# Kernel optimization log

Measured on AMD Instinct MI355X. Metric: run time of the kernel, lower is better.

The kernel has to match this reference:

```python
import jax, jax.numpy as jnp
import numpy as np

NUM_NODES = 256
IN_FEAT = 64
HIDDEN = 512
N_CLASSES = 2
BATCH = 256


def setup_inputs() -> dict:
    key = jax.random.key(0)
    ks = jax.random.split(key, 10)
    return {
        "z": jax.random.normal(ks[0], (BATCH, 1, NUM_NODES, NUM_NODES), dtype=jnp.float32),
        "node_emb": jax.random.normal(ks[1], (NUM_NODES, IN_FEAT), dtype=jnp.float32),
        "w1": jax.random.normal(ks[2], (IN_FEAT, HIDDEN), dtype=jnp.float32) * (1.0 / np.sqrt(IN_FEAT)),
        "b1": jnp.zeros((HIDDEN,), dtype=jnp.float32),
        "w2": jax.random.normal(ks[3], (HIDDEN, HIDDEN), dtype=jnp.float32) * (1.0 / np.sqrt(HIDDEN)),
        "b2": jnp.zeros((HIDDEN,), dtype=jnp.float32),
        "w3": jax.random.normal(ks[4], (HIDDEN, HIDDEN), dtype=jnp.float32) * (1.0 / np.sqrt(HIDDEN)),
        "b3": jnp.zeros((HIDDEN,), dtype=jnp.float32),
        "fcw": jax.random.normal(ks[5], (HIDDEN, N_CLASSES), dtype=jnp.float32) * (1.0 / np.sqrt(HIDDEN)),
        "fcb": jnp.zeros((N_CLASSES,), dtype=jnp.float32),
    }


def reference(z, node_emb, w1, b1, w2, b2, w3, b3, fcw, fcb):
    # z: (B, 1, N, N) latent interpreted as weighted adjacency
    z_sq = jnp.squeeze(z, axis=1)                         # (B, N, N)
    A = jax.nn.sigmoid(z_sq)
    A = (A + jnp.swapaxes(A, 1, 2)) * 0.5                  # symmetrize
    A_hat = A + jnp.eye(A.shape[-1], dtype=A.dtype)[None]  # add self loops
    D_hat = jnp.sum(A_hat, axis=2) + 1e-6                  # (B, N) degrees
    d_inv_sqrt = D_hat ** -0.5
    # norm_A = D^{-1/2} A_hat D^{-1/2} via row/col scaling (same math as diag bmm)
    norm_A = A_hat * d_inv_sqrt[:, :, None] * d_inv_sqrt[:, None, :]

    X = jnp.broadcast_to(node_emb[None], (z.shape[0],) + node_emb.shape)  # (B, N, F)
    H1 = jax.nn.relu(jnp.einsum('bij,bjh->bih', norm_A, X @ w1 + b1))
    H2 = jax.nn.relu(jnp.einsum('bij,bjh->bih', norm_A, H1 @ w2 + b2))
    H3 = jax.nn.relu(jnp.einsum('bij,bjh->bih', norm_A, H2 @ w3 + b3))
    graph_emb = jnp.mean(H3, axis=1)                       # (B, H)
    logits = graph_emb @ fcw + fcb                         # (B, n_classes)
    return logits
```

## Files before the change

kernel.cpp:

```cpp
#include <hip/hip_runtime.h>
#include <stdint.h>

#define B_ 256
#define N_ 256
#define F_ 64
#define H_ 512

typedef _Float16 f16;
typedef _Float16 f16x8 __attribute__((ext_vector_type(8)));
typedef _Float16 f16x4 __attribute__((ext_vector_type(4)));
typedef float    f32x4 __attribute__((ext_vector_type(4)));

__device__ __forceinline__ float sigmoidf_(float x) {
    return 1.0f / (1.0f + __expf(-x));
}

__global__ __launch_bounds__(256) void k_sums(const float* __restrict__ z,
                                              f16* __restrict__ S,
                                              float* __restrict__ R,
                                              float* __restrict__ Cpart) {
    int b = blockIdx.y, c = blockIdx.x;
    int tid = threadIdx.x, lane = tid & 63, w = tid >> 6;
    float colacc[4] = {0.f, 0.f, 0.f, 0.f};
    for (int r = 0; r < 16; r++) {
        int i = c * 64 + w * 16 + r;
        size_t base = ((size_t)(b * N_ + i)) * N_;
        float4 v = *(const float4*)(z + base + lane * 4);
        float s0 = sigmoidf_(v.x), s1 = sigmoidf_(v.y),
              s2 = sigmoidf_(v.z), s3 = sigmoidf_(v.w);
        f16x4 sv = { (f16)s0, (f16)s1, (f16)s2, (f16)s3 };
        *(f16x4*)(S + base + lane * 4) = sv;
        colacc[0] += s0; colacc[1] += s1; colacc[2] += s2; colacc[3] += s3;
        float rs = s0 + s1 + s2 + s3;
        for (int off = 32; off; off >>= 1) rs += __shfl_down(rs, off, 64);
        if (lane == 0) R[b * N_ + i] = rs;
    }
    __shared__ float cbuf[4][N_];
    #pragma unroll
    for (int k = 0; k < 4; k++) cbuf[w][lane * 4 + k] = colacc[k];
    __syncthreads();
    float s4 = cbuf[0][tid] + cbuf[1][tid] + cbuf[2][tid] + cbuf[3][tid];
    Cpart[((size_t)c * B_ + b) * N_ + tid] = s4;
}

__global__ __launch_bounds__(256) void k_norma3(const f16* __restrict__ S,
                                                const float* __restrict__ R,
                                                const float* __restrict__ Cpart,
                                                f16* __restrict__ nA) {
    __shared__ f16 T0[128 * 129];
    __shared__ f16 T1[128 * 129];
    __shared__ float Dv[N_];
    int b = blockIdx.y, t = blockIdx.x;
    int tid = threadIdx.x;
    const f16* Sb = S + (size_t)b * N_ * N_;
    f16* Ab = nA + (size_t)b * N_ * N_;

    float cs = Cpart[(size_t)b * N_ + tid]
             + Cpart[((size_t)B_ + b) * N_ + tid]
             + Cpart[((size_t)2 * B_ + b) * N_ + tid]
             + Cpart[((size_t)3 * B_ + b) * N_ + tid];
    Dv[tid] = rsqrtf(1.0f + 1e-6f + 0.5f * (R[b * N_ + tid] + cs));

    auto stage = [&](const f16* src, f16* dst) {
        #pragma unroll
        for (int it = 0; it < 8; it++) {
            int u = it * 256 + tid;
            int r = u >> 4, c8 = (u & 15) * 8;
            *(f16x8*)&dst[r * 129 + c8] = *(const f16x8*)&src[(size_t)r * N_ + c8];
        }
    };
    if (t == 0)      stage(Sb, T0);
    else if (t == 1) stage(Sb + 128 * N_ + 128, T0);
    else           { stage(Sb + 128, T0); stage(Sb + (size_t)128 * N_, T1); }
    __syncthreads();

    auto emit = [&](const f16* Dir, const f16* Mir, int i0, int j0) {
        #pragma unroll
        for (int it = 0; it < 8; it++) {
            int il = it * 16 + (tid >> 4), jl8 = (tid & 15) * 8;
            float di = Dv[i0 + il];
            f16x8 d = *(const f16x8*)&Dir[il * 129 + jl8];
            f16x8 o;
            #pragma unroll
            for (int k = 0; k < 8; k++) {
                float v = 0.5f * ((float)d[k] + (float)Mir[(jl8 + k) * 129 + il]);
                if (i0 + il == j0 + jl8 + k) v += 1.0f;
                o[k] = (f16)(v * di * Dv[j0 + jl8 + k]);
            }
            *(f16x8*)&Ab[(size_t)(i0 + il) * N_ + j0 + jl8] = o;
        }
    };
    if (t == 0)      emit(T0, T0, 0, 0);
    else if (t == 1) emit(T0, T0, 128, 128);
    else           { emit(T0, T1, 0, 128); emit(T1, T0, 128, 0); }
}

__global__ __launch_bounds__(256) void k_prep(const float* __restrict__ ne,
                                              const float* __restrict__ w1,
                                              const float* __restrict__ b1,
                                              const float* __restrict__ w2,
                                              const float* __restrict__ w3,
                                              f16* __restrict__ XW1t,
                                              f16* __restrict__ w2t,
                                              f16* __restrict__ w3t) {
    int bid = blockIdx.x;
    if (bid < 512) {
        int h = bid, node = threadIdx.x;
        float s = b1[h];
        #pragma unroll 8
        for (int k = 0; k < F_; k++) s += ne[node * F_ + k] * w1[k * H_ + h];
        XW1t[h * N_ + node] = (f16)s;
    } else {
        int idx4 = bid - 512;
        int which = idx4 >> 10;
        const float* src = which ? w3 : w2;
        f16* dst = which ? w3t : w2t;
        int idx = (idx4 & 1023) * 256 + threadIdx.x;
        int k = idx >> 9, n = idx & 511;
        dst[n * H_ + k] = (f16)src[k * H_ + n];
    }
}

template <int KDIM, int MODE>
__global__ __launch_bounds__(256, 4) void k_gemm(const f16* __restrict__ A, long aBatch,
                                                 const f16* __restrict__ Bt, long bBatch,
                                                 f16* __restrict__ Out,
                                                 const float* __restrict__ bias,
                                                 float* __restrict__ gp) {
    __shared__ f16 As[128 * 64];
    __shared__ f16 Bs[128 * 64];
    const int tid  = threadIdx.x;
    const int lane = tid & 63, wave = tid >> 6;
    const int wm = wave >> 1, wn = wave & 1;

    const int lin = blockIdx.x;
    const int xcd = lin & 7, q = lin >> 3;
    const int n_t = q & 3, p = q >> 2;
    const int grp = xcd * 64 + p;
    const int b   = grp >> 1, m_t = grp & 1;
    const int m0 = m_t * 128, n0 = n_t * 128;

    const f16* Ab = A + (size_t)b * aBatch;
    const f16* Bb = Bt + (size_t)b * bBatch;

    f32x4 acc[4][4];
    #pragma unroll
    for (int i = 0; i < 4; i++)
        #pragma unroll
        for (int j = 0; j < 4; j++)
            #pragma unroll
            for (int r = 0; r < 4; r++) acc[i][j][r] = 0.0f;

    const int lr = lane >> 3;
    const int kc = (lane & 7) ^ lr;

    const int ln15 = lane & 15;

    for (int kk = 0; kk < KDIM; kk += 64) {
        #pragma unroll
        for (int c = 0; c < 4; c++) {
            int chunk = wave * 4 + c;
            int row = chunk * 8 + lr;
            __builtin_amdgcn_global_load_lds(
                (__attribute__((address_space(1))) void*)(Ab + (size_t)(m0 + row) * KDIM + kk + kc * 8),
                (__attribute__((address_space(3))) void*)(&As[chunk * 512]), 16, 0, 0);
            __builtin_amdgcn_global_load_lds(
                (__attribute__((address_space(1))) void*)(Bb + (size_t)(n0 + row) * KDIM + kk + kc * 8),
                (__attribute__((address_space(3))) void*)(&Bs[chunk * 512]), 16, 0, 0);
        }
        __syncthreads();

        #pragma unroll
        for (int ks = 0; ks < 2; ks++) {
            const int rkc = ks * 4 + (lane >> 4);
            f16x8 aF[4];
            #pragma unroll
            for (int t = 0; t < 4; t++) {
                int ra = wm * 64 + t * 16 + ln15;
                aF[t] = *(const f16x8*)&As[(ra * 8 + (rkc ^ (ra & 7))) * 8];
            }
            #pragma unroll
            for (int h2 = 0; h2 < 2; h2++) {
                f16x8 bF[2];
                #pragma unroll
                for (int t = 0; t < 2; t++) {
                    int rb = wn * 64 + (h2 * 2 + t) * 16 + ln15;
                    bF[t] = *(const f16x8*)&Bs[(rb * 8 + (rkc ^ (rb & 7))) * 8];
                }
                #pragma unroll
                for (int mt = 0; mt < 4; mt++)
                    #pragma unroll
                    for (int t = 0; t < 2; t++)
                        acc[mt][h2 * 2 + t] = __builtin_amdgcn_mfma_f32_16x16x32_f16(aF[mt], bF[t], acc[mt][h2 * 2 + t], 0, 0, 0);
            }
        }
        __syncthreads();
    }

    const int quad = lane >> 4;
    if (MODE == 0) {
        f16* Ob = Out + (size_t)b * (N_ * H_);
        #pragma unroll
        for (int mt = 0; mt < 4; mt++) {
            int node = m0 + wm * 64 + mt * 16 + quad * 4;
            #pragma unroll
            for (int nt = 0; nt < 4; nt++) {
                int h = n0 + wn * 64 + nt * 16 + ln15;
                #pragma unroll
                for (int rr = 0; rr < 4; rr++) {
                    float v = acc[mt][nt][rr];
                    v = v > 0.f ? v : 0.f;
                    Ob[(size_t)(node + rr) * H_ + h] = (f16)v;
                }
            }
        }
    }
}

template <int REDUCE>
__global__ __launch_bounds__(512, 2) void k_fused(const f16* __restrict__ Hin,
                                                  const f16* __restrict__ Wt,
                                                  const float* __restrict__ bias,
                                                  const f16* __restrict__ nA,
                                                  f16* __restrict__ Hout,
                                                  float* __restrict__ gp) {
    __shared__ f16 As[2][16384];
    __shared__ f16 WU[32768];

    const int tid  = threadIdx.x;
    const int lane = tid & 63, wave = tid >> 6;
    const int ln15 = lane & 15, quad = lane >> 4;
    const int wm = wave >> 1, wn = wave & 1;

    const int lin = blockIdx.x;
    const int xcd = lin & 7, p = lin >> 3;
    const int grp = xcd * 128 + p;
    const int b = grp >> 2, hc = grp & 3;

    const f16* Hb = Hin + (size_t)b * (N_ * H_);
    const f16* Ab = nA + (size_t)b * (N_ * N_);
    const f16* Wc = Wt + (size_t)(hc * 128) * H_;

    const int lr = lane >> 3;
    const int kc = (lane & 7) ^ lr;

    auto stage1 = [&](int buf, int kt) {
        #pragma unroll
        for (int c = 0; c < 4; c++) {
            int chunk = wave * 4 + c;
            int row = chunk * 8 + lr;
            __builtin_amdgcn_global_load_lds(
                (__attribute__((address_space(1))) void*)(Hb + (size_t)row * H_ + kt * 64 + kc * 8),
                (__attribute__((address_space(3))) void*)(&As[buf][chunk * 512]), 16, 0, 0);
        }
        #pragma unroll
        for (int c = 0; c < 2; c++) {
            int chunk = wave * 2 + c;
            int row = chunk * 8 + lr;
            __builtin_amdgcn_global_load_lds(
                (__attribute__((address_space(1))) void*)(Wc + (size_t)row * H_ + kt * 64 + kc * 8),
                (__attribute__((address_space(3))) void*)(&WU[buf * 8192 + chunk * 512]), 16, 0, 0);
        }
    };
    auto stage2 = [&](int buf, int jt) {
        #pragma unroll
        for (int c = 0; c < 4; c++) {
            int chunk = wave * 4 + c;
            int row = chunk * 8 + lr;
            __builtin_amdgcn_global_load_lds(
                (__attribute__((address_space(1))) void*)(Ab + (size_t)row * N_ + jt * 64 + kc * 8),
                (__attribute__((address_space(3))) void*)(&As[buf][chunk * 512]), 16, 0, 0);
        }
    };

    f32x4 acc[4][4];
    #pragma unroll
    for (int i = 0; i < 4; i++)
        #pragma unroll
        for (int j = 0; j < 4; j++)
            #pragma unroll
            for (int r = 0; r < 4; r++) acc[i][j][r] = 0.0f;

    stage1(0, 0);
    __syncthreads();
    for (int kt = 0; kt < 8; ++kt) {
        if (kt < 7) stage1((kt + 1) & 1, kt + 1);
        else        stage2(0, 0);
        const int buf = kt & 1;
        #pragma unroll
        for (int ks = 0; ks < 2; ks++) {
            const int rkc = ks * 4 + quad;
            f16x8 aF[4], bF[4];
            #pragma unroll
            for (int t = 0; t < 4; t++) {
                int ra = wm * 64 + t * 16 + ln15;
                aF[t] = *(const f16x8*)&As[buf][(ra * 8 + (rkc ^ (ra & 7))) * 8];
            }
            #pragma unroll
            for (int t = 0; t < 4; t++) {
                int rb = wn * 64 + t * 16 + ln15;
                bF[t] = *(const f16x8*)&WU[buf * 8192 + (rb * 8 + (rkc ^ (rb & 7))) * 8];
            }
            #pragma unroll
            for (int mt = 0; mt < 4; mt++)
                #pragma unroll
                for (int nt = 0; nt < 4; nt++)
                    acc[mt][nt] = __builtin_amdgcn_mfma_f32_16x16x32_f16(aF[mt], bF[nt], acc[mt][nt], 0, 0, 0);
        }
        __syncthreads();
    }

    #pragma unroll
    for (int nt = 0; nt < 4; nt++) {
        int hl = wn * 64 + nt * 16 + ln15;
        float bv = bias[hc * 128 + hl];
        #pragma unroll
        for (int mt = 0; mt < 4; mt++) {
            int j = wm * 64 + mt * 16 + quad * 4;
            int slot = (j >> 3) ^ (hl & 7);
            f16x4 v;
            #pragma unroll
            for (int rr = 0; rr < 4; rr++) v[rr] = (f16)(acc[mt][nt][rr] + bv);
            *(f16x4*)&WU[hl * 256 + slot * 8 + (j & 7)] = v;
        }
    }
    __syncthreads();

    #pragma unroll
    for (int i = 0; i < 4; i++)
        #pragma unroll
        for (int j = 0; j < 4; j++)
            #pragma unroll
            for (int r = 0; r < 4; r++) acc[i][j][r] = 0.0f;

    for (int jt = 0; jt < 4; ++jt) {
        if (jt < 3) stage2((jt + 1) & 1, jt + 1);
        const int buf = jt & 1;
        #pragma unroll
        for (int ks = 0; ks < 2; ks++) {
            const int rkc = ks * 4 + quad;
            f16x8 aF[4], bF[4];
            #pragma unroll
            for (int t = 0; t < 4; t++) {
                int ra = wm * 64 + t * 16 + ln15;
                aF[t] = *(const f16x8*)&As[buf][(ra * 8 + (rkc ^ (ra & 7))) * 8];
            }
            #pragma unroll
            for (int t = 0; t < 4; t++) {
                int rb = wn * 64 + t * 16 + ln15;
                int g = jt * 8 + rkc;
                bF[t] = *(const f16x8*)&WU[rb * 256 + (g ^ (rb & 7)) * 8];
            }
            #pragma unroll
            for (int mt = 0; mt < 4; mt++)
                #pragma unroll
                for (int nt = 0; nt < 4; nt++)
                    acc[mt][nt] = __builtin_amdgcn_mfma_f32_16x16x32_f16(aF[mt], bF[nt], acc[mt][nt], 0, 0, 0);
        }
        __syncthreads();
    }

    if (REDUCE == 0) {
        f16* Ob = Hout + (size_t)b * (N_ * H_);
        #pragma unroll
        for (int mt = 0; mt < 4; mt++) {
            int node = wm * 64 + mt * 16 + quad * 4;
            #pragma unroll
            for (int nt = 0; nt < 4; nt++) {
                int hg = hc * 128 + wn * 64 + nt * 16 + ln15;
                #pragma unroll
                for (int rr = 0; rr < 4; rr++) {
                    float v = acc[mt][nt][rr];
                    v = v > 0.f ? v : 0.f;
                    Ob[(size_t)(node + rr) * H_ + hg] = (f16)v;
                }
            }
        }
    } else {
        float part[4];
        #pragma unroll
        for (int nt = 0; nt < 4; nt++) {
            float s = 0.f;
            #pragma unroll
            for (int mt = 0; mt < 4; mt++)
                #pragma unroll
                for (int rr = 0; rr < 4; rr++) {
                    float v = acc[mt][nt][rr];
                    s += (v > 0.f ? v : 0.f);
                }
            s += __shfl_down(s, 32, 64);
            s += __shfl_down(s, 16, 64);
            part[nt] = s;
        }
        float* red = (float*)&As[0][0];
        if (quad == 0) {
            #pragma unroll
            for (int nt = 0; nt < 4; nt++)
                red[wave * 64 + nt * 16 + ln15] = part[nt];
        }
        __syncthreads();
        if (tid < 128) {
            int wnl = tid >> 6, cl = tid & 63;
            float g = red[(0 * 2 + wnl) * 64 + cl] + red[(1 * 2 + wnl) * 64 + cl]
                    + red[(2 * 2 + wnl) * 64 + cl] + red[(3 * 2 + wnl) * 64 + cl];
            gp[(size_t)b * H_ + hc * 128 + tid] = g;
        }
    }
}

__global__ __launch_bounds__(256) void k_logits(const float* __restrict__ gp,
                                                const float* __restrict__ fcw,
                                                const float* __restrict__ fcb,
                                                float* __restrict__ out) {
    int b = blockIdx.x, tid = threadIdx.x;
    const float* g = gp + (size_t)b * H_;
    float g0 = g[tid];
    float g1 = g[tid + 256];
    float p0 = g0 * fcw[tid * 2 + 0] + g1 * fcw[(tid + 256) * 2 + 0];
    float p1 = g0 * fcw[tid * 2 + 1] + g1 * fcw[(tid + 256) * 2 + 1];
    for (int off = 32; off; off >>= 1) {
        p0 += __shfl_down(p0, off, 64);
        p1 += __shfl_down(p1, off, 64);
    }
    __shared__ float r0[4], r1[4];
    int lane = tid & 63, w = tid >> 6;
    if (lane == 0) { r0[w] = p0; r1[w] = p1; }
    __syncthreads();
    const float inv = 1.0f / N_;
    if (tid == 0) out[b * 2 + 0] = (r0[0] + r0[1] + r0[2] + r0[3]) * inv + fcb[0];
    if (tid == 1) out[b * 2 + 1] = (r1[0] + r1[1] + r1[2] + r1[3]) * inv + fcb[1];
}

extern "C" void kernel_launch(void* const* d_in, const int* in_sizes, int n_in,
                              void* d_out, int out_size, void* d_ws, size_t ws_size,
                              hipStream_t stream) {
    const float* z   = (const float*)d_in[0];
    const float* ne  = (const float*)d_in[1];
    const float* w1  = (const float*)d_in[2];
    const float* b1  = (const float*)d_in[3];
    const float* w2  = (const float*)d_in[4];
    const float* b2  = (const float*)d_in[5];
    const float* w3  = (const float*)d_in[6];
    const float* b3  = (const float*)d_in[7];
    const float* fcw = (const float*)d_in[8];
    const float* fcb = (const float*)d_in[9];
    float* out = (float*)d_out;

    char* ws = (char*)d_ws;
    f16*   T     = (f16*)(ws + 0);
    float* R     = (float*)(ws + 0);
    float* Cpart = (float*)(ws + 262144);
    f16*   nA    = (f16*)(ws + 67108864);
    f16*   Hh    = (f16*)(ws + 100663296);
    f16*   S     = (f16*)(ws + 100663296);
    float* gpart = (float*)(ws + 100663296);
    f16*   XW1t  = (f16*)(ws + 167772160);
    f16*   w2t   = (f16*)(ws + 168034304);
    f16*   w3t   = (f16*)(ws + 168558592);

    k_sums  <<<dim3(4, B_), 256, 0, stream>>>(z, S, R, Cpart);
    k_norma3<<<dim3(3, B_), 256, 0, stream>>>(S, R, Cpart, nA);
    k_prep  <<<2560,        256, 0, stream>>>(ne, w1, b1, w2, w3, XW1t, w2t, w3t);

    k_gemm<256, 0><<<2048, 256, 0, stream>>>(nA, 65536, XW1t, 0, Hh, nullptr, nullptr);
    k_fused<0><<<1024, 512, 0, stream>>>(Hh, w2t, b2, nA, T, nullptr);
    k_fused<1><<<1024, 512, 0, stream>>>(T, w3t, b3, nA, nullptr, gpart);

    k_logits<<<B_, 256, 0, stream>>>(gpart, fcw, fcb, out);
}
```

Baseline: 320.8 us.

## Load W and normalized-A fragments directly from global into registers, prefetching next tile

The weight tile and the normalized adjacency operand are no longer staged through LDS. Each wave now loads its MFMA fragments straight from global memory into registers, double-buffered one tile ahead, and wave priority is raised around the MFMA blocks. This cuts LDS traffic and removes the per-iteration barrier in the aggregation loop. The costs are more VGPR pressure under launch_bounds(512,2) and uncoalesced 16-byte per-lane global reads that get duplicated across waves sharing rows.

```diff
diff --git a/kernel.cpp b/kernel.cpp
--- a/kernel.cpp
+++ b/kernel.cpp
@@ -225,7 +225,7 @@
                                                   f16* __restrict__ Hout,
                                                   float* __restrict__ gp) {
     __shared__ f16 As[2][16384];
-    __shared__ f16 WU[32768];
+    __shared__ f16 Ut[32768];
 
     const int tid  = threadIdx.x;
     const int lane = tid & 63, wave = tid >> 6;
@@ -244,7 +244,7 @@
     const int lr = lane >> 3;
     const int kc = (lane & 7) ^ lr;
 
-    auto stage1 = [&](int buf, int kt) {
+    auto stageA = [&](int buf, int kt) {
         #pragma unroll
         for (int c = 0; c < 4; c++) {
             int chunk = wave * 4 + c;
@@ -253,24 +253,24 @@
                 (__attribute__((address_space(1))) void*)(Hb + (size_t)row * H_ + kt * 64 + kc * 8),
                 (__attribute__((address_space(3))) void*)(&As[buf][chunk * 512]), 16, 0, 0);
         }
-        #pragma unroll
-        for (int c = 0; c < 2; c++) {
-            int chunk = wave * 2 + c;
-            int row = chunk * 8 + lr;
-            __builtin_amdgcn_global_load_lds(
-                (__attribute__((address_space(1))) void*)(Wc + (size_t)row * H_ + kt * 64 + kc * 8),
-                (__attribute__((address_space(3))) void*)(&WU[buf * 8192 + chunk * 512]), 16, 0, 0);
-        }
     };
-    auto stage2 = [&](int buf, int jt) {
-        #pragma unroll
-        for (int c = 0; c < 4; c++) {
-            int chunk = wave * 4 + c;
-            int row = chunk * 8 + lr;
-            __builtin_amdgcn_global_load_lds(
-                (__attribute__((address_space(1))) void*)(Ab + (size_t)row * N_ + jt * 64 + kc * 8),
-                (__attribute__((address_space(3))) void*)(&As[buf][chunk * 512]), 16, 0, 0);
-        }
+    auto loadW = [&](f16x8* d, int kt) {
+        #pragma unroll
+        for (int ks = 0; ks < 2; ks++)
+            #pragma unroll
+            for (int t = 0; t < 4; t++) {
+                int rb = wn * 64 + t * 16 + ln15;
+                d[ks * 4 + t] = *(const f16x8*)(Wc + (size_t)rb * H_ + kt * 64 + (ks * 4 + quad) * 8);
+            }
+    };
+    auto loadA2 = [&](f16x8* d, int jt) {
+        #pragma unroll
+        for (int ks = 0; ks < 2; ks++)
+            #pragma unroll
+            for (int t = 0; t < 4; t++) {
+                int ra = wm * 64 + t * 16 + ln15;
+                d[ks * 4 + t] = *(const f16x8*)(Ab + (size_t)ra * N_ + jt * 64 + (ks * 4 + quad) * 8);
+            }
     };
 
     f32x4 acc[4][4];
@@ -281,34 +281,41 @@
             #pragma unroll
             for (int r = 0; r < 4; r++) acc[i][j][r] = 0.0f;
 
-    stage1(0, 0);
+    f16x8 bW0[8];
+    loadW(bW0, 0);
+    stageA(0, 0);
     __syncthreads();
     for (int kt = 0; kt < 8; ++kt) {
-        if (kt < 7) stage1((kt + 1) & 1, kt + 1);
-        else        stage2(0, 0);
         const int buf = kt & 1;
+        if (kt < 7) stageA(buf ^ 1, kt + 1);
+        f16x8 bW1[8];
+        if (kt < 7) loadW(bW1, kt + 1);
+        __builtin_amdgcn_s_setprio(1);
         #pragma unroll
         for (int ks = 0; ks < 2; ks++) {
             const int rkc = ks * 4 + quad;
-            f16x8 aF[4], bF[4];
+            f16x8 aF[4];
             #pragma unroll
             for (int t = 0; t < 4; t++) {
                 int ra = wm * 64 + t * 16 + ln15;
                 aF[t] = *(const f16x8*)&As[buf][(ra * 8 + (rkc ^ (ra & 7))) * 8];
             }
             #pragma unroll
-            for (int t = 0; t < 4; t++) {
-                int rb = wn * 64 + t * 16 + ln15;
-                bF[t] = *(const f16x8*)&WU[buf * 8192 + (rb * 8 + (rkc ^ (rb & 7))) * 8];
-            }
-            #pragma unroll
             for (int mt = 0; mt < 4; mt++)
                 #pragma unroll
                 for (int nt = 0; nt < 4; nt++)
-                    acc[mt][nt] = __builtin_amdgcn_mfma_f32_16x16x32_f16(aF[mt], bF[nt], acc[mt][nt], 0, 0, 0);
+                    acc[mt][nt] = __builtin_amdgcn_mfma_f32_16x16x32_f16(aF[mt], bW0[ks * 4 + nt], acc[mt][nt], 0, 0, 0);
+        }
+        __builtin_amdgcn_s_setprio(0);
+        if (kt < 7) {
+            #pragma unroll
+            for (int i = 0; i < 8; i++) bW0[i] = bW1[i];
         }
         __syncthreads();
     }
+
+    f16x8 aN0[8];
+    loadA2(aN0, 0);
 
     #pragma unroll
     for (int nt = 0; nt < 4; nt++) {
@@ -321,7 +328,7 @@
             f16x4 v;
             #pragma unroll
             for (int rr = 0; rr < 4; rr++) v[rr] = (f16)(acc[mt][nt][rr] + bv);
-            *(f16x4*)&WU[hl * 256 + slot * 8 + (j & 7)] = v;
+            *(f16x4*)&Ut[hl * 256 + slot * 8 + (j & 7)] = v;
         }
     }
     __syncthreads();
@@ -334,30 +341,30 @@
             for (int r = 0; r < 4; r++) acc[i][j][r] = 0.0f;
 
     for (int jt = 0; jt < 4; ++jt) {
-        if (jt < 3) stage2((jt + 1) & 1, jt + 1);
-        const int buf = jt & 1;
+        f16x8 aN1[8];
+        if (jt < 3) loadA2(aN1, jt + 1);
+        __builtin_amdgcn_s_setprio(1);
         #pragma unroll
         for (int ks = 0; ks < 2; ks++) {
             const int rkc = ks * 4 + quad;
-            f16x8 aF[4], bF[4];
-            #pragma unroll
-            for (int t = 0; t < 4; t++) {
-                int ra = wm * 64 + t * 16 + ln15;
-                aF[t] = *(const f16x8*)&As[buf][(ra * 8 + (rkc ^ (ra & 7))) * 8];
-            }
+            f16x8 bU[4];
             #pragma unroll
             for (int t = 0; t < 4; t++) {
                 int rb = wn * 64 + t * 16 + ln15;
                 int g = jt * 8 + rkc;
-                bF[t] = *(const f16x8*)&WU[rb * 256 + (g ^ (rb & 7)) * 8];
+                bU[t] = *(const f16x8*)&Ut[rb * 256 + ((g ^ (rb & 7)) * 8)];
             }
             #pragma unroll
             for (int mt = 0; mt < 4; mt++)
                 #pragma unroll
                 for (int nt = 0; nt < 4; nt++)
-                    acc[mt][nt] = __builtin_amdgcn_mfma_f32_16x16x32_f16(aF[mt], bF[nt], acc[mt][nt], 0, 0, 0);
-        }
-        __syncthreads();
+                    acc[mt][nt] = __builtin_amdgcn_mfma_f32_16x16x32_f16(aN0[ks * 4 + mt], bU[nt], acc[mt][nt], 0, 0, 0);
+        }
+        __builtin_amdgcn_s_setprio(0);
+        if (jt < 3) {
+            #pragma unroll
+            for (int i = 0; i < 8; i++) aN0[i] = aN1[i];
+        }
     }
 
     if (REDUCE == 0) {
@@ -392,6 +399,7 @@
             s += __shfl_down(s, 16, 64);
             part[nt] = s;
         }
+        __syncthreads();
         float* red = (float*)&As[0][0];
         if (quad == 0) {
             #pragma unroll
```

Measured after the change: 442.8 us. +38.0%, slower.

## Fuse sigmoid/degree sums and normalized adjacency into one per-batch kernel

Applied to the files above, without the earlier changes.

Replaces the two-kernel pipeline (row/column sums writing an f16 sigmoid matrix to global, then a tiled symmetrize-and-normalize kernel) with one 512-thread block per batch that keeps the whole 256x256 f16 sigmoid matrix in LDS (about 132 KB) and emits the normalized adjacency directly. This removes the global round trip of the intermediate S matrix and the partial-sum buffers, plus one launch. The trade-off is one block per graph with a large LDS footprint, only 256 blocks total, and transposed LDS reads with possible bank conflicts. It also adds a __syncthreads before reusing shared memory in the reduction path.

```diff
diff --git a/kernel.cpp b/kernel.cpp
--- a/kernel.cpp
+++ b/kernel.cpp
@@ -9,90 +9,73 @@
 typedef _Float16 f16;
 typedef _Float16 f16x8 __attribute__((ext_vector_type(8)));
 typedef _Float16 f16x4 __attribute__((ext_vector_type(4)));
+typedef _Float16 f16x2 __attribute__((ext_vector_type(2)));
 typedef float    f32x4 __attribute__((ext_vector_type(4)));
 
 __device__ __forceinline__ float sigmoidf_(float x) {
     return 1.0f / (1.0f + __expf(-x));
 }
 
-__global__ __launch_bounds__(256) void k_sums(const float* __restrict__ z,
-                                              f16* __restrict__ S,
-                                              float* __restrict__ R,
-                                              float* __restrict__ Cpart) {
-    int b = blockIdx.y, c = blockIdx.x;
-    int tid = threadIdx.x, lane = tid & 63, w = tid >> 6;
+__global__ __launch_bounds__(512) void k_fsum(const float* __restrict__ z,
+                                              f16* __restrict__ nA) {
+    constexpr int LD = 258;
+    __shared__ f16 T[256 * LD];
+    __shared__ float cpart[8][256];
+    __shared__ float rbuf[256];
+    __shared__ float Dv[256];
+
+    const int b = blockIdx.x;
+    const int tid = threadIdx.x, lane = tid & 63, w = tid >> 6;
+    const float* zb = z + (size_t)b * (N_ * N_);
+
     float colacc[4] = {0.f, 0.f, 0.f, 0.f};
-    for (int r = 0; r < 16; r++) {
-        int i = c * 64 + w * 16 + r;
-        size_t base = ((size_t)(b * N_ + i)) * N_;
-        float4 v = *(const float4*)(z + base + lane * 4);
+    for (int r = 0; r < 32; r++) {
+        int i = w * 32 + r;
+        float4 v = *(const float4*)(zb + (size_t)i * N_ + lane * 4);
         float s0 = sigmoidf_(v.x), s1 = sigmoidf_(v.y),
               s2 = sigmoidf_(v.z), s3 = sigmoidf_(v.w);
-        f16x4 sv = { (f16)s0, (f16)s1, (f16)s2, (f16)s3 };
-        *(f16x4*)(S + base + lane * 4) = sv;
+        f16x2 p0 = { (f16)s0, (f16)s1 }, p1 = { (f16)s2, (f16)s3 };
+        *(f16x2*)&T[i * LD + lane * 4]     = p0;
+        *(f16x2*)&T[i * LD + lane * 4 + 2] = p1;
         colacc[0] += s0; colacc[1] += s1; colacc[2] += s2; colacc[3] += s3;
         float rs = s0 + s1 + s2 + s3;
         for (int off = 32; off; off >>= 1) rs += __shfl_down(rs, off, 64);
-        if (lane == 0) R[b * N_ + i] = rs;
-    }
-    __shared__ float cbuf[4][N_];
-    #pragma unroll
-    for (int k = 0; k < 4; k++) cbuf[w][lane * 4 + k] = colacc[k];
+        if (lane == 0) rbuf[i] = rs;
+    }
+    #pragma unroll
+    for (int k = 0; k < 4; k++) cpart[w][lane * 4 + k] = colacc[k];
     __syncthreads();
-    float s4 = cbuf[0][tid] + cbuf[1][tid] + cbuf[2][tid] + cbuf[3][tid];
-    Cpart[((size_t)c * B_ + b) * N_ + tid] = s4;
-}
-
-__global__ __launch_bounds__(256) void k_norma3(const f16* __restrict__ S,
-                                                const float* __restrict__ R,
-                                                const float* __restrict__ Cpart,
-                                                f16* __restrict__ nA) {
-    __shared__ f16 T0[128 * 129];
-    __shared__ f16 T1[128 * 129];
-    __shared__ float Dv[N_];
-    int b = blockIdx.y, t = blockIdx.x;
-    int tid = threadIdx.x;
-    const f16* Sb = S + (size_t)b * N_ * N_;
-    f16* Ab = nA + (size_t)b * N_ * N_;
-
-    float cs = Cpart[(size_t)b * N_ + tid]
-             + Cpart[((size_t)B_ + b) * N_ + tid]
-             + Cpart[((size_t)2 * B_ + b) * N_ + tid]
-             + Cpart[((size_t)3 * B_ + b) * N_ + tid];
-    Dv[tid] = rsqrtf(1.0f + 1e-6f + 0.5f * (R[b * N_ + tid] + cs));
-
-    auto stage = [&](const f16* src, f16* dst) {
-        #pragma unroll
-        for (int it = 0; it < 8; it++) {
-            int u = it * 256 + tid;
-            int r = u >> 4, c8 = (u & 15) * 8;
-            *(f16x8*)&dst[r * 129 + c8] = *(const f16x8*)&src[(size_t)r * N_ + c8];
-        }
-    };
-    if (t == 0)      stage(Sb, T0);
-    else if (t == 1) stage(Sb + 128 * N_ + 128, T0);
-    else           { stage(Sb + 128, T0); stage(Sb + (size_t)128 * N_, T1); }
+
+    if (tid < 256) {
+        float cs = 0.f;
+        #pragma unroll
+        for (int ww = 0; ww < 8; ww++) cs += cpart[ww][tid];
+        Dv[tid] = rsqrtf(1.0f + 1e-6f + 0.5f * (rbuf[tid] + cs));
+    }
     __syncthreads();
 
-    auto emit = [&](const f16* Dir, const f16* Mir, int i0, int j0) {
-        #pragma unroll
-        for (int it = 0; it < 8; it++) {
-            int il = it * 16 + (tid >> 4), jl8 = (tid & 15) * 8;
-            float di = Dv[i0 + il];
-            f16x8 d = *(const f16x8*)&Dir[il * 129 + jl8];
-            f16x8 o;
-            #pragma unroll
-            for (int k = 0; k < 8; k++) {
-                float v = 0.5f * ((float)d[k] + (float)Mir[(jl8 + k) * 129 + il]);
-                if (i0 + il == j0 + jl8 + k) v += 1.0f;
-                o[k] = (f16)(v * di * Dv[j0 + jl8 + k]);
-            }
-            *(f16x8*)&Ab[(size_t)(i0 + il) * N_ + j0 + jl8] = o;
-        }
-    };
-    if (t == 0)      emit(T0, T0, 0, 0);
-    else if (t == 1) emit(T0, T0, 128, 128);
-    else           { emit(T0, T1, 0, 128); emit(T1, T0, 128, 0); }
+    const int j8 = (tid & 31) * 8;
+    float dj[8];
+    #pragma unroll
+    for (int k = 0; k < 8; k++) dj[k] = Dv[j8 + k];
+    f16* Ob = nA + (size_t)b * (N_ * N_);
+    for (int it = 0; it < 16; it++) {
+        int i = it * 16 + (tid >> 5);
+        float di = Dv[i];
+        f16x2 dd[4];
+        #pragma unroll
+        for (int c = 0; c < 4; c++)
+            dd[c] = *(const f16x2*)&T[i * LD + j8 + c * 2];
+        f16x8 o;
+        #pragma unroll
+        for (int k = 0; k < 8; k++) {
+            float sij = (float)dd[k >> 1][k & 1];
+            float v = 0.5f * (sij + (float)T[(j8 + k) * LD + i]);
+            if (i == j8 + k) v += 1.0f;
+            o[k] = (f16)(v * di * dj[k]);
+        }
+        *(f16x8*)&Ob[(size_t)i * N_ + j8] = o;
+    }
 }
 
 __global__ __launch_bounds__(256) void k_prep(const float* __restrict__ ne,
@@ -349,7 +332,7 @@
             for (int t = 0; t < 4; t++) {
                 int rb = wn * 64 + t * 16 + ln15;
                 int g = jt * 8 + rkc;
-                bF[t] = *(const f16x8*)&WU[rb * 256 + (g ^ (rb & 7)) * 8];
+                bF[t] = *(const f16x8*)&WU[rb * 256 + ((g ^ (rb & 7)) * 8)];
             }
             #pragma unroll
             for (int mt = 0; mt < 4; mt++)
@@ -392,6 +375,7 @@
             s += __shfl_down(s, 16, 64);
             part[nt] = s;
         }
+        __syncthreads();
         float* red = (float*)&As[0][0];
         if (quad == 0) {
             #pragma unroll
@@ -448,19 +432,15 @@
 
     char* ws = (char*)d_ws;
     f16*   T     = (f16*)(ws + 0);
-    float* R     = (float*)(ws + 0);
-    float* Cpart = (float*)(ws + 262144);
     f16*   nA    = (f16*)(ws + 67108864);
     f16*   Hh    = (f16*)(ws + 100663296);
-    f16*   S     = (f16*)(ws + 100663296);
     float* gpart = (float*)(ws + 100663296);
     f16*   XW1t  = (f16*)(ws + 167772160);
     f16*   w2t   = (f16*)(ws + 168034304);
     f16*   w3t   = (f16*)(ws + 168558592);
 
-    k_sums  <<<dim3(4, B_), 256, 0, stream>>>(z, S, R, Cpart);
-    k_norma3<<<dim3(3, B_), 256, 0, stream>>>(S, R, Cpart, nA);
-    k_prep  <<<2560,        256, 0, stream>>>(ne, w1, b1, w2, w3, XW1t, w2t, w3t);
+    k_fsum<<<256, 512, 0, stream>>>(z, nA);
+    k_prep<<<2560, 256, 0, stream>>>(ne, w1, b1, w2, w3, XW1t, w2t, w3t);
 
     k_gemm<256, 0><<<2048, 256, 0, stream>>>(nA, 65536, XW1t, 0, Hh, nullptr, nullptr);
     k_fused<0><<<1024, 512, 0, stream>>>(Hh, w2t, b2, nA, T, nullptr);
```

Result: no change. 315.1 us (-1.8%).
